# Performance work log

Measured on AMD Instinct MI355X. Metric: run time of the kernel, lower is better.

Reference implementation:

```python
import jax, jax.numpy as jnp
import numpy as np

LN_EPS = 1e-5

def _layer_norm(x, w, b):
    mu = jnp.mean(x, axis=-1, keepdims=True)
    var = jnp.mean(jnp.square(x - mu), axis=-1, keepdims=True)
    return (x - mu) * jax.lax.rsqrt(var + LN_EPS) * w + b

def setup_inputs() -> dict:
    key = jax.random.key(0)
    ks = jax.random.split(key, 8)
    B, NODES, D = 32, 202, 64
    return {
        "embeddings": jax.random.normal(ks[0], (B, NODES, D), dtype=jnp.float32),
        "ln_w": jnp.ones((D,), jnp.float32),
        "ln_b": jnp.zeros((D,), jnp.float32),
        "W1_w": jax.random.normal(ks[1], (D, D), jnp.float32) * 0.05,
        "W1_b": jax.random.normal(ks[2], (D,), jnp.float32) * 0.05,
        "W2_w": jax.random.normal(ks[3], (D, D), jnp.float32) * 0.05,
        "W2_b": jax.random.normal(ks[4], (D,), jnp.float32) * 0.05,
        "a1_w": jax.random.normal(ks[5], (3 * D,), jnp.float32) * 0.05,
        "a1_b": jax.random.normal(ks[6], (1,), jnp.float32) * 0.05,
        "a2_w": jax.random.normal(ks[7], (3 * D,), jnp.float32) * 0.05,
        "a2_b": jax.random.normal(jax.random.fold_in(key, 99), (1,), jnp.float32) * 0.05,
    }

def reference(embeddings, ln_w, ln_b, W1_w, W1_b, W2_w, W2_b, a1_w, a1_b, a2_w, a2_b):
    # embeddings: [B, 2+N, D]; dropout p=0 (eval) -> identity
    emb = _layer_norm(embeddings, ln_w, ln_b)
    uid0 = emb[:, 0, :]          # [B, D]
    iid0 = emb[:, 1, :]          # [B, D]
    iatt = emb[:, 2:, :]         # [B, N, D]
    ua = uid0[:, None, :] * iatt  # [B, N, D]
    # value[b,i,j,:] = LN(ua[b,i] * ua[b,j])  -- the big [B,N,N,D] tensor
    value = _layer_norm(ua[:, :, None, :] * ua[:, None, :, :], ln_w, ln_b)

    def head(Ww, Wb, aw, ab):
        # Linear W applied to expanded query/key/iid collapses to per-row projections;
        # a([wq; wk; wiid]) decomposes additively across the three concat blocks.
        wua = ua @ Ww.T + Wb                  # [B, N, D]  (shared by query rows and key cols)
        wiid = iid0 @ Ww.T + Wb               # [B, D]
        aq, ak, ai = jnp.split(aw, 3)
        sq = wua @ aq                         # [B, N]  query contribution (index i)
        sk = wua @ ak                         # [B, N]  key contribution (index j)
        si = wiid @ ai                        # [B]
        scores = sq[:, :, None] + sk[:, None, :] + si[:, None, None] + ab[0]  # [B,N,N]
        scores = jax.nn.leaky_relu(scores)    # negative_slope=0.01 (torch default)
        alphas = jax.nn.softmax(scores, axis=-1)
        # original sums over dim=-2 (index i), softmax was over j -- kept faithfully
        return jnp.einsum('bij,bijd->bjd', alphas, value)  # [B, N, D]

    att1 = head(W1_w, W1_b, a1_w, a1_b)
    att2 = head(W2_w, W2_b, a2_w, a2_b)
    att_value = (att1 + att2) * 0.5           # [B, N, D]
    ui = (uid0 * iid0)[:, None, :]            # [B, 1, D]
    em_out = jnp.concatenate([ui, att_value], axis=1)  # [B, N+1, D]
    return jax.nn.leaky_relu(em_out)
```

## Files before the change

### kernel.cpp

```cpp
#include <hip/hip_runtime.h>
#include <hip/hip_bf16.h>

#define LN_EPS 1e-5f
#define BB 32
#define NI 200
#define NIP 208
#define DD 64

typedef __attribute__((ext_vector_type(8))) short bf16x8;
typedef __attribute__((ext_vector_type(4))) short bf16x4;
typedef __attribute__((ext_vector_type(4))) float f32x4;

__device__ __forceinline__ float leaky(float x) { return fmaxf(x, 0.01f * x); }
__device__ __forceinline__ short f2bf(float x) {
  __hip_bfloat16 h = __float2bfloat16(x);
  return *reinterpret_cast<short*>(&h);
}
__device__ __forceinline__ float bf2fs(short s) {
  unsigned u = ((unsigned)(unsigned short)s) << 16;
  return __uint_as_float(u);
}
__device__ __forceinline__ bf16x8 sq8(bf16x8 a) {
  bf16x8 r;
#pragma unroll
  for (int k = 0; k < 8; k++) { float f = bf2fs(a[k]); r[k] = f2bf(f * f); }
  return r;
}

#define WS_SC 0
#define WS_T  (WS_SC + BB*NIP*4)
#define WS_CR (WS_T + BB*2)
#define WS_UB (WS_CR + 8)

__device__ __forceinline__ void reduce2(float& a, float& b) {
#pragma unroll
  for (int m = 1; m < 64; m <<= 1) { a += __shfl_xor(a, m, 64); b += __shfl_xor(b, m, 64); }
}
__device__ __forceinline__ void reduce4(float& a, float& b, float& c, float& d) {
#pragma unroll
  for (int m = 1; m < 64; m <<= 1) {
    a += __shfl_xor(a, m, 64); b += __shfl_xor(b, m, 64);
    c += __shfl_xor(c, m, 64); d += __shfl_xor(d, m, 64);
  }
}
__device__ __forceinline__ float reduce1(float a) {
#pragma unroll
  for (int m = 1; m < 64; m <<= 1) a += __shfl_xor(a, m, 64);
  return a;
}
__device__ __forceinline__ void rmax2(float& a, float& b) {
#pragma unroll
  for (int m = 1; m < 64; m <<= 1) {
    a = fmaxf(a, __shfl_xor(a, m, 64));
    b = fmaxf(b, __shfl_xor(b, m, 64));
  }
}

__global__ void __launch_bounds__(256) gat_kX(const float* __restrict__ emb,
                                              const float* __restrict__ lw,
                                              const float* __restrict__ lb,
                                              const float* __restrict__ W1,
                                              const float* __restrict__ W1b,
                                              const float* __restrict__ W2,
                                              const float* __restrict__ W2b,
                                              const float* __restrict__ a1,
                                              const float* __restrict__ a2,
                                              float* __restrict__ ws,
                                              float* __restrict__ out) {
  int b = blockIdx.y, tid = threadIdx.x, wv = tid >> 6, lane = tid & 63;
  int node = blockIdx.x * 4 + wv;
  __shared__ float v_sh[4][64];
  __shared__ float vi_sh[2][64];
  __shared__ float iid_sh[64];

  float w = lw[lane], bi = lb[lane];
  auto lnrow = [&](int n) -> float {
    float x = emb[(size_t)(b * 202 + n) * 64 + lane];
    float s = x, s2 = x * x;
    reduce2(s, s2);
    float mu = s * (1.f / 64);
    float var = fmaxf(s2 * (1.f / 64) - mu * mu, 0.f);
    return (x - mu) * rsqrtf(var + LN_EPS) * w + bi;
  };
  float u = lnrow(0);
  float y = 0.f;
  if (node >= 1 && node <= 201) y = lnrow(node);
  if (node == 1) {
    iid_sh[lane] = y;
    out[(size_t)(b * 201) * 64 + lane] = leaky(u * y);
  }
  if (wv == 0) {
    float p0 = 0, p1 = 0;
#pragma unroll 8
    for (int d = 0; d < 64; d++) {
      float x = W1[d * 64 + lane];
      p0 = fmaf(x, a1[d], p0); p1 = fmaf(x, a1[64 + d], p1);
    }
    v_sh[0][lane] = p0; v_sh[1][lane] = p1;
  } else if (wv == 1) {
    float p0 = 0, p1 = 0;
#pragma unroll 8
    for (int d = 0; d < 64; d++) {
      float x = W2[d * 64 + lane];
      p0 = fmaf(x, a2[d], p0); p1 = fmaf(x, a2[64 + d], p1);
    }
    v_sh[2][lane] = p0; v_sh[3][lane] = p1;
  } else if (blockIdx.x == 0 && wv == 2) {
    float p = 0;
#pragma unroll 8
    for (int d = 0; d < 64; d++) p = fmaf(W1[d * 64 + lane], a1[128 + d], p);
    vi_sh[0][lane] = p;
  } else if (blockIdx.x == 0 && wv == 3) {
    float p = 0;
#pragma unroll 8
    for (int d = 0; d < 64; d++) p = fmaf(W2[d * 64 + lane], a2[128 + d], p);
    vi_sh[1][lane] = p;
  }
  __syncthreads();

  if (node >= 2 && node <= 201) {
    int i = node - 2;
    float a = u * y;
    ((unsigned short*)(ws + WS_UB))[(size_t)(b * NI + i) * 64 + lane] =
        (unsigned short)f2bf(a);
    float p0 = a * v_sh[0][lane], p1 = a * v_sh[1][lane];
    float p2 = a * v_sh[2][lane], p3 = a * v_sh[3][lane];
    reduce4(p0, p1, p2, p3);
    if (lane == 0) {
      f32x4 sc = {p0, p1, p2, p3};
      *(f32x4*)(ws + WS_SC + (size_t)(b * NIP + i) * 4) = sc;
    }
  }
  if (blockIdx.x == 0 && wv == 0) {
    float q0 = iid_sh[lane] * vi_sh[0][lane];
    float q1 = iid_sh[lane] * vi_sh[1][lane];
    reduce2(q0, q1);
    if (lane == 0) { ws[WS_T + b * 2] = q0; ws[WS_T + b * 2 + 1] = q1; }
  }
  if (blockIdx.x == 0 && b == 0 && wv == 1) {
    float c0 = reduce1(W1b[lane] * a1[lane]);
    float c1 = reduce1(W1b[lane] * a1[64 + lane]);
    float c2 = reduce1(W1b[lane] * a1[128 + lane]);
    float c3 = reduce1(W2b[lane] * a2[lane]);
    float c4 = reduce1(W2b[lane] * a2[64 + lane]);
    float c5 = reduce1(W2b[lane] * a2[128 + lane]);
    if (lane == 0) {
      ws[WS_CR + 0] = c0; ws[WS_CR + 1] = c1; ws[WS_CR + 2] = c2;
      ws[WS_CR + 3] = c3; ws[WS_CR + 4] = c4; ws[WS_CR + 5] = c5;
    }
  }
}

__global__ void __launch_bounds__(256) gat_kY(const float* __restrict__ ws,
                                              const float* __restrict__ lw,
                                              const float* __restrict__ lb,
                                              const float* __restrict__ a1b,
                                              const float* __restrict__ a2b,
                                              float* __restrict__ out) {
  int b = blockIdx.y, jt = blockIdx.x, tid = threadIdx.x;
  int wv = tid >> 6, lane = tid & 63, q = lane >> 4, col = lane & 15;
  __shared__ __align__(16) short sUA[13 * 2 * 64 * 8];
  __shared__ __align__(16) short sUAT[7 * 4 * 64 * 8];
  __shared__ __align__(16) short sG[7 * 64 * 8];
  __shared__ float sPart[4][2][16];
  __shared__ float sST[NIP][6];
  __shared__ float skv[2][NIP];
  __shared__ float wmx[4][2];

  const unsigned short* uwb =
      (const unsigned short*)(ws + WS_UB) + (size_t)b * NI * 64;

  for (int idx = tid; idx < 13 * 2 * 64; idx += 256) {
    int itile = idx >> 7, rem = idx & 127, kh = rem >> 6, ln = rem & 63;
    int node = itile * 16 + (ln & 15);
    int dbase = kh * 32 + (ln >> 4) * 8;
    bf16x8 pk;
    if (node < NI) pk = *(const bf16x8*)(uwb + node * 64 + dbase);
    else {
#pragma unroll
      for (int k = 0; k < 8; k++) pk[k] = 0;
    }
    *(bf16x8*)(sUA + idx * 8) = pk;
  }
  {
    int d = tid & 63, ir = tid >> 6;
#pragma unroll
    for (int p = 0; p < 7; p++) {
      int i0 = p * 32 + ir * 8;
      bf16x8 pk;
#pragma unroll
      for (int u = 0; u < 8; u++)
        pk[u] = (i0 + u < NI) ? (short)uwb[(i0 + u) * 64 + d] : (short)0;
      int off = ((p * 4 + (d >> 4)) * 64 + ((d & 15) + 16 * ir)) * 8;
      *(bf16x8*)(sUAT + off) = pk;
    }
  }
  ((int*)(sG + (6 * 64 + 32) * 8))[tid] = 0;

  float c0 = ws[WS_CR + 0], c1 = ws[WS_CR + 1], c2 = ws[WS_CR + 2];
  float c3 = ws[WS_CR + 3], c4 = ws[WS_CR + 4], c5 = ws[WS_CR + 5];
  float t1 = ws[WS_T + b * 2] + c2 + a1b[0];
  float t2 = ws[WS_T + b * 2 + 1] + c5 + a2b[0];
  float base1 = 0, base2 = 0;
  if (tid < NIP) {
    f32x4 sc = *(const f32x4*)(ws + WS_SC + (size_t)(b * NIP + tid) * 4);
    base1 = sc.x + c0 + t1;
    base2 = sc.z + c3 + t2;
    skv[0][tid] = sc.y + c1;
    skv[1][tid] = sc.w + c4;
  }
  __syncthreads();

  float m1 = (tid < NI) ? skv[0][tid] : -3e38f;
  float m2 = (tid < NI) ? skv[1][tid] : -3e38f;
  rmax2(m1, m2);
  if (lane == 0) { wmx[wv][0] = m1; wmx[wv][1] = m2; }
  __syncthreads();

  if (tid < NIP) {
    float rm1 = 0, iv1 = 0, rm2 = 0, iv2 = 0, b1 = 0, b2 = 0;
    if (tid < NI) {
      float mx1 = fmaxf(fmaxf(wmx[0][0], wmx[1][0]), fmaxf(wmx[2][0], wmx[3][0]));
      float mx2 = fmaxf(fmaxf(wmx[0][1], wmx[1][1]), fmaxf(wmx[2][1], wmx[3][1]));
      b1 = base1; b2 = base2;
      rm1 = leaky(base1 + mx1);
      rm2 = leaky(base2 + mx2);
      float d1 = 0, d2 = 0;
#pragma unroll 4
      for (int j = 0; j < NI; j++) {
        float s1 = base1 + skv[0][j];
        d1 += __expf(fmaxf(s1, 0.01f * s1) - rm1);
        float s2 = base2 + skv[1][j];
        d2 += __expf(fmaxf(s2, 0.01f * s2) - rm2);
      }
      iv1 = 1.0f / d1; iv2 = 1.0f / d2;
    }
    sST[tid][0] = b1; sST[tid][1] = rm1; sST[tid][2] = iv1;
    sST[tid][3] = b2; sST[tid][4] = rm2; sST[tid][5] = iv2;
  }
  __syncthreads();

  bf16x8 bf0 = *(bf16x8*)(sUA + ((jt * 2 + 0) * 64 + lane) * 8);
  bf16x8 bf1 = *(bf16x8*)(sUA + ((jt * 2 + 1) * 64 + lane) * 8);
  bf16x8 b2f0 = sq8(bf0), b2f1 = sq8(bf1);
  int jglob = jt * 16 + col;
  float skj1 = skv[0][jglob], skj2 = skv[1][jglob];
  float mpart = 0.f, spart = 0.f;

  for (int it = wv; it < 13; it += 4) {
    bf16x8 af0 = *(bf16x8*)(sUA + ((it * 2 + 0) * 64 + lane) * 8);
    bf16x8 af1 = *(bf16x8*)(sUA + ((it * 2 + 1) * 64 + lane) * 8);
    bf16x8 a2f0 = sq8(af0), a2f1 = sq8(af1);
    f32x4 s = {0, 0, 0, 0}, t = {0, 0, 0, 0};
    s = __builtin_amdgcn_mfma_f32_16x16x32_bf16(af0, bf0, s, 0, 0, 0);
    s = __builtin_amdgcn_mfma_f32_16x16x32_bf16(af1, bf1, s, 0, 0, 0);
    t = __builtin_amdgcn_mfma_f32_16x16x32_bf16(a2f0, b2f0, t, 0, 0, 0);
    t = __builtin_amdgcn_mfma_f32_16x16x32_bf16(a2f1, b2f1, t, 0, 0, 0);
    bf16x4 gp;
#pragma unroll
    for (int r = 0; r < 4; r++) {
      int i = it * 16 + q * 4 + r;
      float bb1 = sST[i][0], rr1 = sST[i][1], vv1 = sST[i][2];
      float bb2 = sST[i][3], rr2 = sST[i][4], vv2 = sST[i][5];
      float mu = s[r] * (1.f / 64);
      float var = fmaxf(t[r] * (1.f / 64) - mu * mu, 0.f);
      float inv = rsqrtf(var + LN_EPS);
      float sc1 = bb1 + skj1;
      float e1 = __expf(fmaxf(sc1, 0.01f * sc1) - rr1) * vv1;
      float sc2 = bb2 + skj2;
      float e2 = __expf(fmaxf(sc2, 0.01f * sc2) - rr2) * vv2;
      float c = 0.5f * (e1 + e2);
      float g = c * inv;
      mpart = fmaf(g, mu, mpart);
      spart += c;
      gp[r] = f2bf(g);
    }
    int kl = (it & 1) * 16 + q * 4;
    int off = ((it >> 1) * 64 + (col + 16 * (kl >> 3))) * 8 + (kl & 7);
    *(bf16x4*)(sG + off) = gp;
  }
  mpart += __shfl_xor(mpart, 16, 64); mpart += __shfl_xor(mpart, 32, 64);
  spart += __shfl_xor(spart, 16, 64); spart += __shfl_xor(spart, 32, 64);
  if (lane < 16) { sPart[wv][0][lane] = mpart; sPart[wv][1][lane] = spart; }
  __syncthreads();

  f32x4 acc = {0, 0, 0, 0};
#pragma unroll
  for (int kt = 0; kt < 7; kt++) {
    bf16x8 ga = *(bf16x8*)(sG + (kt * 64 + lane) * 8);
    bf16x8 ub = *(bf16x8*)(sUAT + ((kt * 4 + wv) * 64 + lane) * 8);
    acc = __builtin_amdgcn_mfma_f32_16x16x32_bf16(ga, ub, acc, 0, 0, 0);
  }
  int d = wv * 16 + col;
  float w = lw[d], bia = lb[d];
#pragma unroll
  for (int r = 0; r < 4; r++) {
    int jl = q * 4 + r, jg = jt * 16 + jl;
    if (jg < NI) {
      float m = sPart[0][0][jl] + sPart[1][0][jl] + sPart[2][0][jl] + sPart[3][0][jl];
      float S = sPart[0][1][jl] + sPart[1][1][jl] + sPart[2][1][jl] + sPart[3][1][jl];
      float uajd = bf2fs((short)uwb[jg * 64 + d]);
      float att = w * (uajd * acc[r] - m) + bia * S;
      out[(size_t)(b * 201 + 1 + jg) * 64 + d] = leaky(att);
    }
  }
}

extern "C" void kernel_launch(void* const* d_in, const int* in_sizes, int n_in,
                              void* d_out, int out_size, void* d_ws, size_t ws_size,
                              hipStream_t stream) {
  const float* emb = (const float*)d_in[0];
  const float* lw  = (const float*)d_in[1];
  const float* lb  = (const float*)d_in[2];
  const float* W1  = (const float*)d_in[3];
  const float* W1b = (const float*)d_in[4];
  const float* W2  = (const float*)d_in[5];
  const float* W2b = (const float*)d_in[6];
  const float* a1  = (const float*)d_in[7];
  const float* a1b = (const float*)d_in[8];
  const float* a2  = (const float*)d_in[9];
  const float* a2b = (const float*)d_in[10];
  float* ws = (float*)d_ws;
  float* out = (float*)d_out;

  gat_kX<<<dim3(51, BB), dim3(256), 0, stream>>>(emb, lw, lb, W1, W1b, W2, W2b,
                                                 a1, a2, ws, out);
  gat_kY<<<dim3(13, BB), dim3(256), 0, stream>>>(ws, lw, lb, a1b, a2b, out);
}
```

Baseline: 100.7 us.

## Fuse prep and attention kernels into one cooperative kernel with grid sync

The two launches are merged into a single cooperative kernel of 416 blocks. The first phase computes LayerNorm rows and writes ua in bf16 straight into MFMA-ready swizzled layouts (node-major and d-major), and the second phase runs after a grid-wide sync. This removes one kernel launch gap, replaces the strided transpose gather in the attention phase with contiguous vector copies, and reads ua_j from shared memory. In exchange it adds a grid barrier, and every block now recomputes the W·a projections.

```diff
diff --git a/kernel.cpp b/kernel.cpp
--- a/kernel.cpp
+++ b/kernel.cpp
@@ -1,5 +1,8 @@
 #include <hip/hip_runtime.h>
 #include <hip/hip_bf16.h>
+#include <hip/hip_cooperative_groups.h>
+
+namespace cg = cooperative_groups;
 
 #define LN_EPS 1e-5f
 #define BB 32
@@ -30,7 +33,8 @@
 #define WS_SC 0
 #define WS_T  (WS_SC + BB*NIP*4)
 #define WS_CR (WS_T + BB*2)
-#define WS_UB (WS_CR + 8)
+#define WS_NM (WS_CR + 8)
+#define WS_DM (WS_NM + BB*6656)
 
 __device__ __forceinline__ void reduce2(float& a, float& b) {
 #pragma unroll
@@ -56,39 +60,28 @@
   }
 }
 
-__global__ void __launch_bounds__(256) gat_kX(const float* __restrict__ emb,
-                                              const float* __restrict__ lw,
-                                              const float* __restrict__ lb,
-                                              const float* __restrict__ W1,
-                                              const float* __restrict__ W1b,
-                                              const float* __restrict__ W2,
-                                              const float* __restrict__ W2b,
-                                              const float* __restrict__ a1,
-                                              const float* __restrict__ a2,
-                                              float* __restrict__ ws,
-                                              float* __restrict__ out) {
-  int b = blockIdx.y, tid = threadIdx.x, wv = tid >> 6, lane = tid & 63;
-  int node = blockIdx.x * 4 + wv;
-  __shared__ float v_sh[4][64];
-  __shared__ float vi_sh[2][64];
-  __shared__ float iid_sh[64];
-
-  float w = lw[lane], bi = lb[lane];
-  auto lnrow = [&](int n) -> float {
-    float x = emb[(size_t)(b * 202 + n) * 64 + lane];
-    float s = x, s2 = x * x;
-    reduce2(s, s2);
-    float mu = s * (1.f / 64);
-    float var = fmaxf(s2 * (1.f / 64) - mu * mu, 0.f);
-    return (x - mu) * rsqrtf(var + LN_EPS) * w + bi;
-  };
-  float u = lnrow(0);
-  float y = 0.f;
-  if (node >= 1 && node <= 201) y = lnrow(node);
-  if (node == 1) {
-    iid_sh[lane] = y;
-    out[(size_t)(b * 201) * 64 + lane] = leaky(u * y);
-  }
+#define SM_UA   0
+#define SM_UAT  26624
+#define SM_G    55296
+#define SM_PART 62464
+#define SM_ST   62976
+#define SM_SKV  67968
+#define SM_WMX  69632
+
+__global__ void __launch_bounds__(256) gat_fused(
+    const float* __restrict__ emb, const float* __restrict__ lw,
+    const float* __restrict__ lb, const float* __restrict__ W1,
+    const float* __restrict__ W1b, const float* __restrict__ W2,
+    const float* __restrict__ W2b, const float* __restrict__ a1,
+    const float* __restrict__ a1b, const float* __restrict__ a2,
+    const float* __restrict__ a2b, float* __restrict__ ws,
+    float* __restrict__ out) {
+  __shared__ __align__(16) char smem[69664];
+  int tid = threadIdx.x, wv = tid >> 6, lane = tid & 63;
+
+  float* v_sh  = (float*)smem;
+  float* vi_sh = (float*)smem + 256;
+
   if (wv == 0) {
     float p0 = 0, p1 = 0;
 #pragma unroll 8
@@ -96,7 +89,7 @@
       float x = W1[d * 64 + lane];
       p0 = fmaf(x, a1[d], p0); p1 = fmaf(x, a1[64 + d], p1);
     }
-    v_sh[0][lane] = p0; v_sh[1][lane] = p1;
+    v_sh[lane] = p0; v_sh[64 + lane] = p1;
   } else if (wv == 1) {
     float p0 = 0, p1 = 0;
 #pragma unroll 8
@@ -104,40 +97,16 @@
       float x = W2[d * 64 + lane];
       p0 = fmaf(x, a2[d], p0); p1 = fmaf(x, a2[64 + d], p1);
     }
-    v_sh[2][lane] = p0; v_sh[3][lane] = p1;
-  } else if (blockIdx.x == 0 && wv == 2) {
-    float p = 0;
+    v_sh[128 + lane] = p0; v_sh[192 + lane] = p1;
+  } else if (wv == 2) {
+    float p0 = 0, p1 = 0;
 #pragma unroll 8
-    for (int d = 0; d < 64; d++) p = fmaf(W1[d * 64 + lane], a1[128 + d], p);
-    vi_sh[0][lane] = p;
-  } else if (blockIdx.x == 0 && wv == 3) {
-    float p = 0;
-#pragma unroll 8
-    for (int d = 0; d < 64; d++) p = fmaf(W2[d * 64 + lane], a2[128 + d], p);
-    vi_sh[1][lane] = p;
-  }
-  __syncthreads();
-
-  if (node >= 2 && node <= 201) {
-    int i = node - 2;
-    float a = u * y;
-    ((unsigned short*)(ws + WS_UB))[(size_t)(b * NI + i) * 64 + lane] =
-        (unsigned short)f2bf(a);
-    float p0 = a * v_sh[0][lane], p1 = a * v_sh[1][lane];
-    float p2 = a * v_sh[2][lane], p3 = a * v_sh[3][lane];
-    reduce4(p0, p1, p2, p3);
-    if (lane == 0) {
-      f32x4 sc = {p0, p1, p2, p3};
-      *(f32x4*)(ws + WS_SC + (size_t)(b * NIP + i) * 4) = sc;
-    }
-  }
-  if (blockIdx.x == 0 && wv == 0) {
-    float q0 = iid_sh[lane] * vi_sh[0][lane];
-    float q1 = iid_sh[lane] * vi_sh[1][lane];
-    reduce2(q0, q1);
-    if (lane == 0) { ws[WS_T + b * 2] = q0; ws[WS_T + b * 2 + 1] = q1; }
-  }
-  if (blockIdx.x == 0 && b == 0 && wv == 1) {
+    for (int d = 0; d < 64; d++) {
+      p0 = fmaf(W1[d * 64 + lane], a1[128 + d], p0);
+      p1 = fmaf(W2[d * 64 + lane], a2[128 + d], p1);
+    }
+    vi_sh[lane] = p0; vi_sh[64 + lane] = p1;
+  } else if (blockIdx.x == 0) {
     float c0 = reduce1(W1b[lane] * a1[lane]);
     float c1 = reduce1(W1b[lane] * a1[64 + lane]);
     float c2 = reduce1(W1b[lane] * a1[128 + lane]);
@@ -149,94 +118,113 @@
       ws[WS_CR + 3] = c3; ws[WS_CR + 4] = c4; ws[WS_CR + 5] = c5;
     }
   }
-}
-
-__global__ void __launch_bounds__(256) gat_kY(const float* __restrict__ ws,
-                                              const float* __restrict__ lw,
-                                              const float* __restrict__ lb,
-                                              const float* __restrict__ a1b,
-                                              const float* __restrict__ a2b,
-                                              float* __restrict__ out) {
-  int b = blockIdx.y, jt = blockIdx.x, tid = threadIdx.x;
-  int wv = tid >> 6, lane = tid & 63, q = lane >> 4, col = lane & 15;
-  __shared__ __align__(16) short sUA[13 * 2 * 64 * 8];
-  __shared__ __align__(16) short sUAT[7 * 4 * 64 * 8];
-  __shared__ __align__(16) short sG[7 * 64 * 8];
-  __shared__ float sPart[4][2][16];
-  __shared__ float sST[NIP][6];
-  __shared__ float skv[2][NIP];
-  __shared__ float wmx[4][2];
-
-  const unsigned short* uwb =
-      (const unsigned short*)(ws + WS_UB) + (size_t)b * NI * 64;
-
-  for (int idx = tid; idx < 13 * 2 * 64; idx += 256) {
-    int itile = idx >> 7, rem = idx & 127, kh = rem >> 6, ln = rem & 63;
-    int node = itile * 16 + (ln & 15);
-    int dbase = kh * 32 + (ln >> 4) * 8;
-    bf16x8 pk;
-    if (node < NI) pk = *(const bf16x8*)(uwb + node * 64 + dbase);
-    else {
-#pragma unroll
-      for (int k = 0; k < 8; k++) pk[k] = 0;
-    }
-    *(bf16x8*)(sUA + idx * 8) = pk;
-  }
+  __syncthreads();
+
   {
-    int d = tid & 63, ir = tid >> 6;
-#pragma unroll
-    for (int p = 0; p < 7; p++) {
-      int i0 = p * 32 + ir * 8;
-      bf16x8 pk;
-#pragma unroll
-      for (int u = 0; u < 8; u++)
-        pk[u] = (i0 + u < NI) ? (short)uwb[(i0 + u) * 64 + d] : (short)0;
-      int off = ((p * 4 + (d >> 4)) * 64 + ((d & 15) + 16 * ir)) * 8;
-      *(bf16x8*)(sUAT + off) = pk;
-    }
-  }
-  ((int*)(sG + (6 * 64 + 32) * 8))[tid] = 0;
+    float w = lw[lane], bi = lb[lane];
+    auto lnrow = [&](int bb, int n) -> float {
+      float x = emb[(size_t)(bb * 202 + n) * 64 + lane];
+      float s = x, s2 = x * x;
+      reduce2(s, s2);
+      float mu = s * (1.f / 64);
+      float var = fmaxf(s2 * (1.f / 64) - mu * mu, 0.f);
+      return (x - mu) * rsqrtf(var + LN_EPS) * w + bi;
+    };
+    int gw = blockIdx.x * 4 + wv;
+    for (int k = 0; k < 4; k++) {
+      int f = gw + k * 1664;
+      if (f >= BB * 202) break;
+      int b = f / 202, node = f - b * 202;
+      if (node == 0) continue;
+      float u = lnrow(b, 0);
+      float y = lnrow(b, node);
+      if (node == 1) {
+        out[(size_t)(b * 201) * 64 + lane] = leaky(u * y);
+        float q0 = y * vi_sh[lane], q1 = y * vi_sh[64 + lane];
+        reduce2(q0, q1);
+        if (lane == 0) { ws[WS_T + b * 2] = q0; ws[WS_T + b * 2 + 1] = q1; }
+      } else {
+        int i = node - 2, d = lane;
+        float a = u * y;
+        unsigned short ab = (unsigned short)f2bf(a);
+        unsigned short* nm = (unsigned short*)(ws + WS_NM) + (size_t)b * 13312;
+        unsigned short* dm = (unsigned short*)(ws + WS_DM) + (size_t)b * 14336;
+        nm[(((i >> 4) * 128 + (d >> 5) * 64 + ((d >> 3) & 3) * 16 + (i & 15)) << 3)
+           + (d & 7)] = ab;
+        dm[((((i >> 5) * 4 + (d >> 4)) * 64 + ((i >> 3) & 3) * 16 + (d & 15)) << 3)
+           + (i & 7)] = ab;
+        float p0 = a * v_sh[lane],       p1 = a * v_sh[64 + lane];
+        float p2 = a * v_sh[128 + lane], p3 = a * v_sh[192 + lane];
+        reduce4(p0, p1, p2, p3);
+        if (lane == 0) {
+          f32x4 sc = {p0, p1, p2, p3};
+          *(f32x4*)(ws + WS_SC + (size_t)(b * NIP + i) * 4) = sc;
+        }
+      }
+    }
+  }
+
+  cg::this_grid().sync();
+
+  int pb = blockIdx.x & 31, jt = blockIdx.x >> 5;
+  int q = lane >> 4, col = lane & 15;
+  short* sUA  = (short*)(smem + SM_UA);
+  short* sUAT = (short*)(smem + SM_UAT);
+  short* sG   = (short*)(smem + SM_G);
+  float* sPart = (float*)(smem + SM_PART);
+  float* sST   = (float*)(smem + SM_ST);
+  float* skv   = (float*)(smem + SM_SKV);
+  float* wmx   = (float*)(smem + SM_WMX);
+
+  const unsigned short* nm = (const unsigned short*)(ws + WS_NM) + (size_t)pb * 13312;
+  const unsigned short* dm = (const unsigned short*)(ws + WS_DM) + (size_t)pb * 14336;
+  for (int idx = tid; idx < 1664; idx += 256)
+    *(bf16x8*)(sUA + idx * 8) = *(const bf16x8*)(nm + idx * 8);
+  for (int idx = tid; idx < 1792; idx += 256)
+    *(bf16x8*)(sUAT + idx * 8) = *(const bf16x8*)(dm + idx * 8);
+  if (tid < 128) ((int*)sG)[1664 + tid] = 0;
 
   float c0 = ws[WS_CR + 0], c1 = ws[WS_CR + 1], c2 = ws[WS_CR + 2];
   float c3 = ws[WS_CR + 3], c4 = ws[WS_CR + 4], c5 = ws[WS_CR + 5];
-  float t1 = ws[WS_T + b * 2] + c2 + a1b[0];
-  float t2 = ws[WS_T + b * 2 + 1] + c5 + a2b[0];
+  float t1 = ws[WS_T + pb * 2] + c2 + a1b[0];
+  float t2 = ws[WS_T + pb * 2 + 1] + c5 + a2b[0];
   float base1 = 0, base2 = 0;
   if (tid < NIP) {
-    f32x4 sc = *(const f32x4*)(ws + WS_SC + (size_t)(b * NIP + tid) * 4);
+    f32x4 sc = *(const f32x4*)(ws + WS_SC + (size_t)(pb * NIP + tid) * 4);
     base1 = sc.x + c0 + t1;
     base2 = sc.z + c3 + t2;
-    skv[0][tid] = sc.y + c1;
-    skv[1][tid] = sc.w + c4;
-  }
-  __syncthreads();
-
-  float m1 = (tid < NI) ? skv[0][tid] : -3e38f;
-  float m2 = (tid < NI) ? skv[1][tid] : -3e38f;
+    skv[0 * NIP + tid] = sc.y + c1;
+    skv[1 * NIP + tid] = sc.w + c4;
+  }
+  __syncthreads();
+
+  float m1 = (tid < NI) ? skv[0 * NIP + tid] : -3e38f;
+  float m2 = (tid < NI) ? skv[1 * NIP + tid] : -3e38f;
   rmax2(m1, m2);
-  if (lane == 0) { wmx[wv][0] = m1; wmx[wv][1] = m2; }
+  if (lane == 0) { wmx[wv * 2] = m1; wmx[wv * 2 + 1] = m2; }
   __syncthreads();
 
   if (tid < NIP) {
     float rm1 = 0, iv1 = 0, rm2 = 0, iv2 = 0, b1 = 0, b2 = 0;
     if (tid < NI) {
-      float mx1 = fmaxf(fmaxf(wmx[0][0], wmx[1][0]), fmaxf(wmx[2][0], wmx[3][0]));
-      float mx2 = fmaxf(fmaxf(wmx[0][1], wmx[1][1]), fmaxf(wmx[2][1], wmx[3][1]));
+      float mx1 = fmaxf(fmaxf(wmx[0], wmx[2]), fmaxf(wmx[4], wmx[6]));
+      float mx2 = fmaxf(fmaxf(wmx[1], wmx[3]), fmaxf(wmx[5], wmx[7]));
       b1 = base1; b2 = base2;
       rm1 = leaky(base1 + mx1);
       rm2 = leaky(base2 + mx2);
       float d1 = 0, d2 = 0;
 #pragma unroll 4
       for (int j = 0; j < NI; j++) {
-        float s1 = base1 + skv[0][j];
+        float s1 = base1 + skv[0 * NIP + j];
         d1 += __expf(fmaxf(s1, 0.01f * s1) - rm1);
-        float s2 = base2 + skv[1][j];
+        float s2 = base2 + skv[1 * NIP + j];
         d2 += __expf(fmaxf(s2, 0.01f * s2) - rm2);
       }
       iv1 = 1.0f / d1; iv2 = 1.0f / d2;
     }
-    sST[tid][0] = b1; sST[tid][1] = rm1; sST[tid][2] = iv1;
-    sST[tid][3] = b2; sST[tid][4] = rm2; sST[tid][5] = iv2;
+    float* st = sST + tid * 6;
+    st[0] = b1; st[1] = rm1; st[2] = iv1;
+    st[3] = b2; st[4] = rm2; st[5] = iv2;
   }
   __syncthreads();
 
@@ -244,7 +232,7 @@
   bf16x8 bf1 = *(bf16x8*)(sUA + ((jt * 2 + 1) * 64 + lane) * 8);
   bf16x8 b2f0 = sq8(bf0), b2f1 = sq8(bf1);
   int jglob = jt * 16 + col;
-  float skj1 = skv[0][jglob], skj2 = skv[1][jglob];
+  float skj1 = skv[0 * NIP + jglob], skj2 = skv[1 * NIP + jglob];
   float mpart = 0.f, spart = 0.f;
 
   for (int it = wv; it < 13; it += 4) {
@@ -260,15 +248,14 @@
 #pragma unroll
     for (int r = 0; r < 4; r++) {
       int i = it * 16 + q * 4 + r;
-      float bb1 = sST[i][0], rr1 = sST[i][1], vv1 = sST[i][2];
-      float bb2 = sST[i][3], rr2 = sST[i][4], vv2 = sST[i][5];
+      const float* st = sST + i * 6;
       float mu = s[r] * (1.f / 64);
       float var = fmaxf(t[r] * (1.f / 64) - mu * mu, 0.f);
       float inv = rsqrtf(var + LN_EPS);
-      float sc1 = bb1 + skj1;
-      float e1 = __expf(fmaxf(sc1, 0.01f * sc1) - rr1) * vv1;
-      float sc2 = bb2 + skj2;
-      float e2 = __expf(fmaxf(sc2, 0.01f * sc2) - rr2) * vv2;
+      float sc1 = st[0] + skj1;
+      float e1 = __expf(fmaxf(sc1, 0.01f * sc1) - st[1]) * st[2];
+      float sc2 = st[3] + skj2;
+      float e2 = __expf(fmaxf(sc2, 0.01f * sc2) - st[4]) * st[5];
       float c = 0.5f * (e1 + e2);
       float g = c * inv;
       mpart = fmaf(g, mu, mpart);
@@ -281,7 +268,10 @@
   }
   mpart += __shfl_xor(mpart, 16, 64); mpart += __shfl_xor(mpart, 32, 64);
   spart += __shfl_xor(spart, 16, 64); spart += __shfl_xor(spart, 32, 64);
-  if (lane < 16) { sPart[wv][0][lane] = mpart; sPart[wv][1][lane] = spart; }
+  if (lane < 16) {
+    sPart[(wv * 2 + 0) * 16 + lane] = mpart;
+    sPart[(wv * 2 + 1) * 16 + lane] = spart;
+  }
   __syncthreads();
 
   f32x4 acc = {0, 0, 0, 0};
@@ -297,11 +287,14 @@
   for (int r = 0; r < 4; r++) {
     int jl = q * 4 + r, jg = jt * 16 + jl;
     if (jg < NI) {
-      float m = sPart[0][0][jl] + sPart[1][0][jl] + sPart[2][0][jl] + sPart[3][0][jl];
-      float S = sPart[0][1][jl] + sPart[1][1][jl] + sPart[2][1][jl] + sPart[3][1][jl];
-      float uajd = bf2fs((short)uwb[jg * 64 + d]);
+      float m = sPart[0 * 16 + jl] + sPart[2 * 16 + jl] +
+                sPart[4 * 16 + jl] + sPart[6 * 16 + jl];
+      float S = sPart[1 * 16 + jl] + sPart[3 * 16 + jl] +
+                sPart[5 * 16 + jl] + sPart[7 * 16 + jl];
+      int cn = jt * 128 + (d >> 5) * 64 + ((d >> 3) & 3) * 16 + (jg & 15);
+      float uajd = bf2fs(sUA[cn * 8 + (d & 7)]);
       float att = w * (uajd * acc[r] - m) + bia * S;
-      out[(size_t)(b * 201 + 1 + jg) * 64 + d] = leaky(att);
+      out[(size_t)(pb * 201 + 1 + jg) * 64 + d] = leaky(att);
     }
   }
 }
@@ -323,7 +316,9 @@
   float* ws = (float*)d_ws;
   float* out = (float*)d_out;
 
-  gat_kX<<<dim3(51, BB), dim3(256), 0, stream>>>(emb, lw, lb, W1, W1b, W2, W2b,
-                                                 a1, a2, ws, out);
-  gat_kY<<<dim3(13, BB), dim3(256), 0, stream>>>(ws, lw, lb, a1b, a2b, out);
-}
+  void* args[] = {(void*)&emb, (void*)&lw, (void*)&lb, (void*)&W1, (void*)&W1b,
+                  (void*)&W2, (void*)&W2b, (void*)&a1, (void*)&a1b, (void*)&a2,
+                  (void*)&a2b, (void*)&ws, (void*)&out};
+  hipLaunchCooperativeKernel((const void*)gat_fused, dim3(13 * BB), dim3(256),
+                             args, 0, stream);
+}
```

Result: slower. 170.5 us (+69.3%).

## Process two j-tiles per 512-thread block and split softmax stats across halves

Applied to the files above, without the earlier changes.

The second kernel now runs 512 threads per block, and each half handles its own 16-column j tile. This cuts the grid from 13 to 7 blocks per batch and roughly halves the redundant per-block staging of UA/UAT and the softmax denominator precompute. The denominator loop is split so that each head's 200 rows are computed by separate threads, and the final ua value is read from shared memory instead of global. In exchange, the block uses more shared memory (about 77KB), half of the last block sits idle, and occupancy per CU may drop.

```diff
diff --git a/kernel.cpp b/kernel.cpp
--- a/kernel.cpp
+++ b/kernel.cpp
@@ -151,26 +151,39 @@
   }
 }
 
-__global__ void __launch_bounds__(256) gat_kY(const float* __restrict__ ws,
+#define SM_UA   0
+#define SM_UAT  26624
+#define SM_G0   55296
+#define SM_G1   62464
+#define SM_PART 69632
+#define SM_ST   70656
+#define SM_SKV  75648
+#define SM_WMX  77312
+
+__global__ void __launch_bounds__(512) gat_kY(const float* __restrict__ ws,
                                               const float* __restrict__ lw,
                                               const float* __restrict__ lb,
                                               const float* __restrict__ a1b,
                                               const float* __restrict__ a2b,
                                               float* __restrict__ out) {
-  int b = blockIdx.y, jt = blockIdx.x, tid = threadIdx.x;
+  __shared__ __align__(16) char smem[77376];
+  int b = blockIdx.y, bx = blockIdx.x, tid = threadIdx.x;
   int wv = tid >> 6, lane = tid & 63, q = lane >> 4, col = lane & 15;
-  __shared__ __align__(16) short sUA[13 * 2 * 64 * 8];
-  __shared__ __align__(16) short sUAT[7 * 4 * 64 * 8];
-  __shared__ __align__(16) short sG[7 * 64 * 8];
-  __shared__ float sPart[4][2][16];
-  __shared__ float sST[NIP][6];
-  __shared__ float skv[2][NIP];
-  __shared__ float wmx[4][2];
+  int half = wv >> 2, wq = wv & 3;
+
+  short* sUA  = (short*)(smem + SM_UA);
+  short* sUAT = (short*)(smem + SM_UAT);
+  short* sG0  = (short*)(smem + SM_G0);
+  short* sG1  = (short*)(smem + SM_G1);
+  float* sPart = (float*)(smem + SM_PART);
+  float* sST   = (float*)(smem + SM_ST);
+  float* skv   = (float*)(smem + SM_SKV);
+  float* wmx   = (float*)(smem + SM_WMX);
 
   const unsigned short* uwb =
       (const unsigned short*)(ws + WS_UB) + (size_t)b * NI * 64;
 
-  for (int idx = tid; idx < 13 * 2 * 64; idx += 256) {
+  for (int idx = tid; idx < 1664; idx += 512) {
     int itile = idx >> 7, rem = idx & 127, kh = rem >> 6, ln = rem & 63;
     int node = itile * 16 + (ln & 15);
     int dbase = kh * 32 + (ln >> 4) * 8;
@@ -183,9 +196,8 @@
     *(bf16x8*)(sUA + idx * 8) = pk;
   }
   {
-    int d = tid & 63, ir = tid >> 6;
-#pragma unroll
-    for (int p = 0; p < 7; p++) {
+    int d = tid & 63, ir = (tid >> 6) & 3, ph = tid >> 8;
+    for (int p = ph; p < 7; p += 2) {
       int i0 = p * 32 + ir * 8;
       bf16x8 pk;
 #pragma unroll
@@ -195,113 +207,132 @@
       *(bf16x8*)(sUAT + off) = pk;
     }
   }
-  ((int*)(sG + (6 * 64 + 32) * 8))[tid] = 0;
+  if (tid < 128) ((int*)sG0)[1664 + tid] = 0;
+  else if (tid < 256) ((int*)sG1)[1664 + (tid - 128)] = 0;
 
   float c0 = ws[WS_CR + 0], c1 = ws[WS_CR + 1], c2 = ws[WS_CR + 2];
   float c3 = ws[WS_CR + 3], c4 = ws[WS_CR + 4], c5 = ws[WS_CR + 5];
   float t1 = ws[WS_T + b * 2] + c2 + a1b[0];
   float t2 = ws[WS_T + b * 2 + 1] + c5 + a2b[0];
-  float base1 = 0, base2 = 0;
   if (tid < NIP) {
     f32x4 sc = *(const f32x4*)(ws + WS_SC + (size_t)(b * NIP + tid) * 4);
-    base1 = sc.x + c0 + t1;
-    base2 = sc.z + c3 + t2;
-    skv[0][tid] = sc.y + c1;
-    skv[1][tid] = sc.w + c4;
-  }
-  __syncthreads();
-
-  float m1 = (tid < NI) ? skv[0][tid] : -3e38f;
-  float m2 = (tid < NI) ? skv[1][tid] : -3e38f;
+    float* st = sST + tid * 6;
+    if (tid < NI) {
+      st[0] = sc.x + c0 + t1;
+      st[3] = sc.z + c3 + t2;
+    } else { st[0] = 0; st[3] = 0; }
+    st[1] = 0; st[2] = 0; st[4] = 0; st[5] = 0;
+    skv[0 * NIP + tid] = sc.y + c1;
+    skv[1 * NIP + tid] = sc.w + c4;
+  }
+  __syncthreads();
+
+  float m1 = (tid < NI) ? skv[0 * NIP + tid] : -3e38f;
+  float m2 = (tid < NI) ? skv[1 * NIP + tid] : -3e38f;
   rmax2(m1, m2);
-  if (lane == 0) { wmx[wv][0] = m1; wmx[wv][1] = m2; }
-  __syncthreads();
-
-  if (tid < NIP) {
-    float rm1 = 0, iv1 = 0, rm2 = 0, iv2 = 0, b1 = 0, b2 = 0;
-    if (tid < NI) {
-      float mx1 = fmaxf(fmaxf(wmx[0][0], wmx[1][0]), fmaxf(wmx[2][0], wmx[3][0]));
-      float mx2 = fmaxf(fmaxf(wmx[0][1], wmx[1][1]), fmaxf(wmx[2][1], wmx[3][1]));
-      b1 = base1; b2 = base2;
-      rm1 = leaky(base1 + mx1);
-      rm2 = leaky(base2 + mx2);
-      float d1 = 0, d2 = 0;
+  if (lane == 0) { wmx[wv * 2] = m1; wmx[wv * 2 + 1] = m2; }
+  __syncthreads();
+
+  {
+    int sh = -1, si = 0;
+    if (tid < NI) { sh = 0; si = tid; }
+    else if (tid >= 256 && tid < 256 + NI) { sh = 1; si = tid - 256; }
+    if (sh >= 0) {
+      float mx = -3e38f;
+#pragma unroll
+      for (int k = 0; k < 8; k++) mx = fmaxf(mx, wmx[k * 2 + sh]);
+      float* st = sST + si * 6;
+      float base = st[sh * 3];
+      float rm = leaky(base + mx);
+      const float* skh = skv + sh * NIP;
+      float den = 0.f;
 #pragma unroll 4
       for (int j = 0; j < NI; j++) {
-        float s1 = base1 + skv[0][j];
-        d1 += __expf(fmaxf(s1, 0.01f * s1) - rm1);
-        float s2 = base2 + skv[1][j];
-        d2 += __expf(fmaxf(s2, 0.01f * s2) - rm2);
+        float s = base + skh[j];
+        den += __expf(fmaxf(s, 0.01f * s) - rm);
       }
-      iv1 = 1.0f / d1; iv2 = 1.0f / d2;
-    }
-    sST[tid][0] = b1; sST[tid][1] = rm1; sST[tid][2] = iv1;
-    sST[tid][3] = b2; sST[tid][4] = rm2; sST[tid][5] = iv2;
-  }
-  __syncthreads();
-
-  bf16x8 bf0 = *(bf16x8*)(sUA + ((jt * 2 + 0) * 64 + lane) * 8);
-  bf16x8 bf1 = *(bf16x8*)(sUA + ((jt * 2 + 1) * 64 + lane) * 8);
-  bf16x8 b2f0 = sq8(bf0), b2f1 = sq8(bf1);
-  int jglob = jt * 16 + col;
-  float skj1 = skv[0][jglob], skj2 = skv[1][jglob];
-  float mpart = 0.f, spart = 0.f;
-
-  for (int it = wv; it < 13; it += 4) {
-    bf16x8 af0 = *(bf16x8*)(sUA + ((it * 2 + 0) * 64 + lane) * 8);
-    bf16x8 af1 = *(bf16x8*)(sUA + ((it * 2 + 1) * 64 + lane) * 8);
-    bf16x8 a2f0 = sq8(af0), a2f1 = sq8(af1);
-    f32x4 s = {0, 0, 0, 0}, t = {0, 0, 0, 0};
-    s = __builtin_amdgcn_mfma_f32_16x16x32_bf16(af0, bf0, s, 0, 0, 0);
-    s = __builtin_amdgcn_mfma_f32_16x16x32_bf16(af1, bf1, s, 0, 0, 0);
-    t = __builtin_amdgcn_mfma_f32_16x16x32_bf16(a2f0, b2f0, t, 0, 0, 0);
-    t = __builtin_amdgcn_mfma_f32_16x16x32_bf16(a2f1, b2f1, t, 0, 0, 0);
-    bf16x4 gp;
+      st[sh * 3 + 1] = rm;
+      st[sh * 3 + 2] = 1.0f / den;
+    }
+  }
+  __syncthreads();
+
+  int jt = bx * 2 + half;
+  bool act = (jt < 13);
+  short* sGh = half ? sG1 : sG0;
+  float* sPh = sPart + half * 128;
+  float skj1 = 0, skj2 = 0;
+  bf16x8 bf0, bf1, b2f0, b2f1;
+  if (act) {
+    bf0 = *(bf16x8*)(sUA + ((jt * 2 + 0) * 64 + lane) * 8);
+    bf1 = *(bf16x8*)(sUA + ((jt * 2 + 1) * 64 + lane) * 8);
+    b2f0 = sq8(bf0); b2f1 = sq8(bf1);
+    int jglob = jt * 16 + col;
+    skj1 = skv[0 * NIP + jglob]; skj2 = skv[1 * NIP + jglob];
+    float mpart = 0.f, spart = 0.f;
+    for (int it = wq; it < 13; it += 4) {
+      bf16x8 af0 = *(bf16x8*)(sUA + ((it * 2 + 0) * 64 + lane) * 8);
+      bf16x8 af1 = *(bf16x8*)(sUA + ((it * 2 + 1) * 64 + lane) * 8);
+      bf16x8 a2f0 = sq8(af0), a2f1 = sq8(af1);
+      f32x4 s = {0, 0, 0, 0}, t = {0, 0, 0, 0};
+      s = __builtin_amdgcn_mfma_f32_16x16x32_bf16(af0, bf0, s, 0, 0, 0);
+      s = __builtin_amdgcn_mfma_f32_16x16x32_bf16(af1, bf1, s, 0, 0, 0);
+      t = __builtin_amdgcn_mfma_f32_16x16x32_bf16(a2f0, b2f0, t, 0, 0, 0);
+      t = __builtin_amdgcn_mfma_f32_16x16x32_bf16(a2f1, b2f1, t, 0, 0, 0);
+      bf16x4 gp;
+#pragma unroll
+      for (int r = 0; r < 4; r++) {
+        int i = it * 16 + q * 4 + r;
+        const float* st = sST + i * 6;
+        float mu = s[r] * (1.f / 64);
+        float var = fmaxf(t[r] * (1.f / 64) - mu * mu, 0.f);
+        float inv = rsqrtf(var + LN_EPS);
+        float sc1 = st[0] + skj1;
+        float e1 = __expf(fmaxf(sc1, 0.01f * sc1) - st[1]) * st[2];
+        float sc2 = st[3] + skj2;
+        float e2 = __expf(fmaxf(sc2, 0.01f * sc2) - st[4]) * st[5];
+        float c = 0.5f * (e1 + e2);
+        float g = c * inv;
+        mpart = fmaf(g, mu, mpart);
+        spart += c;
+        gp[r] = f2bf(g);
+      }
+      int kl = (it & 1) * 16 + q * 4;
+      int off = ((it >> 1) * 64 + (col + 16 * (kl >> 3))) * 8 + (kl & 7);
+      *(bf16x4*)(sGh + off) = gp;
+    }
+    mpart += __shfl_xor(mpart, 16, 64); mpart += __shfl_xor(mpart, 32, 64);
+    spart += __shfl_xor(spart, 16, 64); spart += __shfl_xor(spart, 32, 64);
+    if (lane < 16) {
+      sPh[(wq * 2 + 0) * 16 + lane] = mpart;
+      sPh[(wq * 2 + 1) * 16 + lane] = spart;
+    }
+  }
+  __syncthreads();
+
+  if (act) {
+    f32x4 acc = {0, 0, 0, 0};
+#pragma unroll
+    for (int kt = 0; kt < 7; kt++) {
+      bf16x8 ga = *(bf16x8*)(sGh + (kt * 64 + lane) * 8);
+      bf16x8 ub = *(bf16x8*)(sUAT + ((kt * 4 + wq) * 64 + lane) * 8);
+      acc = __builtin_amdgcn_mfma_f32_16x16x32_bf16(ga, ub, acc, 0, 0, 0);
+    }
+    int d = wq * 16 + col;
+    float w = lw[d], bia = lb[d];
 #pragma unroll
     for (int r = 0; r < 4; r++) {
-      int i = it * 16 + q * 4 + r;
-      float bb1 = sST[i][0], rr1 = sST[i][1], vv1 = sST[i][2];
-      float bb2 = sST[i][3], rr2 = sST[i][4], vv2 = sST[i][5];
-      float mu = s[r] * (1.f / 64);
-      float var = fmaxf(t[r] * (1.f / 64) - mu * mu, 0.f);
-      float inv = rsqrtf(var + LN_EPS);
-      float sc1 = bb1 + skj1;
-      float e1 = __expf(fmaxf(sc1, 0.01f * sc1) - rr1) * vv1;
-      float sc2 = bb2 + skj2;
-      float e2 = __expf(fmaxf(sc2, 0.01f * sc2) - rr2) * vv2;
-      float c = 0.5f * (e1 + e2);
-      float g = c * inv;
-      mpart = fmaf(g, mu, mpart);
-      spart += c;
-      gp[r] = f2bf(g);
-    }
-    int kl = (it & 1) * 16 + q * 4;
-    int off = ((it >> 1) * 64 + (col + 16 * (kl >> 3))) * 8 + (kl & 7);
-    *(bf16x4*)(sG + off) = gp;
-  }
-  mpart += __shfl_xor(mpart, 16, 64); mpart += __shfl_xor(mpart, 32, 64);
-  spart += __shfl_xor(spart, 16, 64); spart += __shfl_xor(spart, 32, 64);
-  if (lane < 16) { sPart[wv][0][lane] = mpart; sPart[wv][1][lane] = spart; }
-  __syncthreads();
-
-  f32x4 acc = {0, 0, 0, 0};
-#pragma unroll
-  for (int kt = 0; kt < 7; kt++) {
-    bf16x8 ga = *(bf16x8*)(sG + (kt * 64 + lane) * 8);
-    bf16x8 ub = *(bf16x8*)(sUAT + ((kt * 4 + wv) * 64 + lane) * 8);
-    acc = __builtin_amdgcn_mfma_f32_16x16x32_bf16(ga, ub, acc, 0, 0, 0);
-  }
-  int d = wv * 16 + col;
-  float w = lw[d], bia = lb[d];
-#pragma unroll
-  for (int r = 0; r < 4; r++) {
-    int jl = q * 4 + r, jg = jt * 16 + jl;
-    if (jg < NI) {
-      float m = sPart[0][0][jl] + sPart[1][0][jl] + sPart[2][0][jl] + sPart[3][0][jl];
-      float S = sPart[0][1][jl] + sPart[1][1][jl] + sPart[2][1][jl] + sPart[3][1][jl];
-      float uajd = bf2fs((short)uwb[jg * 64 + d]);
-      float att = w * (uajd * acc[r] - m) + bia * S;
-      out[(size_t)(b * 201 + 1 + jg) * 64 + d] = leaky(att);
+      int jl = q * 4 + r, jg = jt * 16 + jl;
+      if (jg < NI) {
+        float m = sPh[0 * 16 + jl] + sPh[2 * 16 + jl] +
+                  sPh[4 * 16 + jl] + sPh[6 * 16 + jl];
+        float S = sPh[1 * 16 + jl] + sPh[3 * 16 + jl] +
+                  sPh[5 * 16 + jl] + sPh[7 * 16 + jl];
+        int cn = jt * 128 + (d >> 5) * 64 + ((d >> 3) & 3) * 16 + (jg & 15);
+        float uajd = bf2fs(sUA[cn * 8 + (d & 7)]);
+        float att = w * (uajd * acc[r] - m) + bia * S;
+        out[(size_t)(b * 201 + 1 + jg) * 64 + d] = leaky(att);
+      }
     }
   }
 }
@@ -325,5 +356,5 @@
 
   gat_kX<<<dim3(51, BB), dim3(256), 0, stream>>>(emb, lw, lb, W1, W1b, W2, W2b,
                                                  a1, a2, ws, out);
-  gat_kY<<<dim3(13, BB), dim3(256), 0, stream>>>(ws, lw, lb, a1b, a2b, out);
-}
+  gat_kY<<<dim3(7, BB), dim3(512), 0, stream>>>(ws, lw, lb, a1b, a2b, out);
+}
```

After: 93.18 us. -7.5%, faster.
